# Kernel tuning notes

Hardware: AMD Instinct MI355X
Metric: run time of the kernel (lower is better)

## Reference

```python
import jax, jax.numpy as jnp
import numpy as np

B, S, D = 16, 2048, 128


def setup_inputs() -> dict:
    key = jax.random.key(0)
    kq, kk, kv, km = jax.random.split(key, 4)
    q = jax.random.normal(kq, (B, S, D), dtype=jnp.float32)
    k = jax.random.normal(kk, (B, S, D), dtype=jnp.float32)
    v = jax.random.normal(kv, (B, S, D), dtype=jnp.float32)
    mask = jax.random.randint(km, (B, S, S), 0, 2, dtype=jnp.int32)
    return {"q": q, "k": k, "v": v, "mask": mask}


def softmax_one(x):
    # repo's softmax_one: subtract max, denominator is 1 + sum(exp)
    x = x - jnp.max(x, axis=-1, keepdims=True)
    e = jnp.exp(x)
    return e / (1.0 + jnp.sum(e, axis=-1, keepdims=True))


def reference(q, k, v, mask):
    d_k = k.shape[-1]
    zero = jnp.zeros((q.shape[0], 1, d_k), dtype=q.dtype)
    # prepend zero 'sink' key/value token along the sequence axis
    k1 = jnp.concatenate([zero, k], axis=1)          # [B, S+1, D]
    v1 = jnp.concatenate([zero, v], axis=1)          # [B, S+1, D]
    scores = jnp.einsum('bqd,bkd->bqk', q, k1) / np.sqrt(d_k)  # [B, S, S+1]
    # F.pad(mask, (1, 0)) pads sink column with 0 -> sink score masked
    m = jnp.pad(mask, ((0, 0), (0, 0), (1, 0)))
    scores = jnp.where(m == 0, jnp.float32(-1e9), scores)
    p_attn = softmax_one(scores)                     # [B, S, S+1]
    out = jnp.einsum('bqk,bkd->bqd', p_attn, v1)     # [B, S, D]
    return (out, p_attn)
```

## Files before the change

kernel.cpp:

```cpp
#include <hip/hip_runtime.h>
#include <hip/hip_bf16.h>

typedef __attribute__((ext_vector_type(8))) __bf16 bf16x8;
typedef __attribute__((ext_vector_type(4))) __bf16 bf16x4;
typedef __attribute__((ext_vector_type(4))) float  f32x4;
typedef float f32x4u __attribute__((ext_vector_type(4), aligned(4)));

#define NB 16
#define NS 2048
#define ND 128
#define QT 64
#define KT 64
#define NKT (NS / KT)
#define SCALE 0.08838834764831845f

#define VMW12() asm volatile("s_waitcnt vmcnt(12)" ::: "memory")
#define VMW8()  asm volatile("s_waitcnt vmcnt(8)"  ::: "memory")
#define VMW4()  asm volatile("s_waitcnt vmcnt(4)"  ::: "memory")
#define SCHED0() __builtin_amdgcn_sched_barrier(0)
#define SBAR()  __builtin_amdgcn_s_barrier()

__device__ __forceinline__ bf16x8 ld8_256(const __bf16* base, int row, int byteInRow) {
    int off = row * 256 + (byteInRow ^ ((row & 7) << 4));
    return *reinterpret_cast<const bf16x8*>(reinterpret_cast<const char*>(base) + off);
}
__device__ __forceinline__ bf16x8 ld8_128(const __bf16* base, int row, int byteInRow) {
    int off = row * 128 + (byteInRow ^ ((row & 7) << 4));
    return *reinterpret_cast<const bf16x8*>(reinterpret_cast<const char*>(base) + off);
}
__device__ __forceinline__ void glds16(const void* g, void* l) {
    __builtin_amdgcn_global_load_lds(
        (const __attribute__((address_space(1))) unsigned int*)g,
        (__attribute__((address_space(3))) unsigned int*)l, 16, 0, 0);
}

__global__ __launch_bounds__(256) void conv_qk(const float* __restrict__ q,
                                               const float* __restrict__ k,
                                               __bf16* __restrict__ qb,
                                               __bf16* __restrict__ kb) {
    size_t i = (size_t)blockIdx.x * 256 + threadIdx.x;
    const float4* qs = (const float4*)q;
    const float4* ks = (const float4*)k;
    float4 a = qs[2 * i], b = qs[2 * i + 1];
    bf16x8 o;
    o[0] = (__bf16)(a.x * SCALE); o[1] = (__bf16)(a.y * SCALE);
    o[2] = (__bf16)(a.z * SCALE); o[3] = (__bf16)(a.w * SCALE);
    o[4] = (__bf16)(b.x * SCALE); o[5] = (__bf16)(b.y * SCALE);
    o[6] = (__bf16)(b.z * SCALE); o[7] = (__bf16)(b.w * SCALE);
    *(bf16x8*)&qb[i * 8] = o;
    a = ks[2 * i]; b = ks[2 * i + 1];
    o[0] = (__bf16)a.x; o[1] = (__bf16)a.y; o[2] = (__bf16)a.z; o[3] = (__bf16)a.w;
    o[4] = (__bf16)b.x; o[5] = (__bf16)b.y; o[6] = (__bf16)b.z; o[7] = (__bf16)b.w;
    *(bf16x8*)&kb[i * 8] = o;
}

__global__ __launch_bounds__(256) void conv_vt(const float* __restrict__ v,
                                               __bf16* __restrict__ vt) {
    __shared__ __bf16 tile[128 * 128];
    const int b = blockIdx.x >> 4, st = blockIdx.x & 15;
    const int s0 = st * 128, t = threadIdx.x;
    const int rlane = t >> 5, cv = (t & 31) * 4;
    #pragma unroll
    for (int it = 0; it < 16; ++it) {
        int s = rlane + it * 8;
        float4 f = *(const float4*)(v + ((size_t)b * NS + s0 + s) * ND + cv);
        bf16x4 h;
        h[0] = (__bf16)f.x; h[1] = (__bf16)f.y; h[2] = (__bf16)f.z; h[3] = (__bf16)f.w;
        *(bf16x4*)&tile[s * 128 + (cv ^ (s & 60))] = h;
    }
    __syncthreads();
    #pragma unroll
    for (int it = 0; it < 16; ++it) {
        int d = rlane + it * 8;
        bf16x4 o;
        #pragma unroll
        for (int e = 0; e < 4; ++e)
            o[e] = tile[(cv + e) * 128 + (d ^ ((cv + e) & 60))];
        *(bf16x4*)&vt[((size_t)b * ND + d) * NS + s0 + cv] = o;
    }
}

__global__ __launch_bounds__(256, 2) void qa_main(
    const __bf16* __restrict__ qb, const __bf16* __restrict__ kb,
    const __bf16* __restrict__ vtb, const int* __restrict__ mg,
    float* __restrict__ outg, float* __restrict__ pg)
{
    __shared__ __align__(16) char bufs[3][KT * ND * 2];
    __shared__ unsigned short bmt[NKT * 256];
    __shared__ __align__(16) __bf16 Ps[4][16 * KT];

    const int bid = blockIdx.x;
    const int lb  = (bid & 7) * 64 + (bid >> 3);
    const int b   = lb >> 5;
    const int q0  = (lb & 31) * QT;
    const int t   = threadIdx.x;
    const int w   = t >> 6;
    const int l15 = t & 15;
    const int g   = (t & 63) >> 4;
    const int myrow = w * 16 + l15;

    const __bf16* kbB  = kb  + (size_t)b * NS * ND;
    const __bf16* vtbB = vtb + (size_t)b * ND * NS;
    const int*    mrow = mg  + (size_t)(b * NS + q0 + myrow) * NS;

    if (t < QT) pg[(size_t)(b * NS + q0 + t) * (size_t)(NS + 1)] = 0.0f;

    bf16x8 qf[4];
    {
        const __bf16* qrow = qb + (size_t)(b * NS + q0 + myrow) * ND;
        #pragma unroll
        for (int kc = 0; kc < 4; ++kc)
            qf[kc] = *(const bf16x8*)(qrow + kc * 32 + g * 8);
    }

    auto stageK = [&](char* buf, int k0) {
        #pragma unroll
        for (int i = 0; i < 4; ++i) {
            int c = i * 256 + t;
            int row = c >> 4, pc = c & 15, lc = pc ^ (row & 7);
            glds16(kbB + (size_t)(k0 + row) * ND + lc * 8, buf + c * 16);
        }
    };
    auto stageV = [&](char* buf, int k0) {
        #pragma unroll
        for (int i = 0; i < 4; ++i) {
            int c = i * 256 + t;
            int d = c >> 3, pc = c & 7, lc = pc ^ (d & 7);
            glds16(vtbB + (size_t)d * NS + k0 + lc * 8, buf + c * 16);
        }
    };

    float mrun = -1e9f, srun = 0.0f;
    int4 mA[4], mB[4];

    stageK(bufs[0], 0);
    stageK(bufs[1], KT);
    #pragma unroll
    for (int c = 0; c < 4; ++c) mA[c] = *(const int4*)(mrow + c * 16 + g * 4);
    VMW8();
    SCHED0(); SBAR(); SCHED0();

    auto stepA = [&](int kt, const int4* mcur, int4* mnxt) {
        if (kt + 2 < NKT) stageK(bufs[(kt + 2) % 3], (kt + 2) * KT);
        if (kt + 1 < NKT) {
            #pragma unroll
            for (int c = 0; c < 4; ++c)
                mnxt[c] = *(const int4*)(mrow + (kt + 1) * KT + c * 16 + g * 4);
        }
        const __bf16* Kbuf = (const __bf16*)bufs[kt % 3];
        f32x4 acc[4];
        #pragma unroll
        for (int c = 0; c < 4; ++c) {
            f32x4 z = {0.f, 0.f, 0.f, 0.f}; acc[c] = z;
            #pragma unroll
            for (int kc = 0; kc < 4; ++kc) {
                bf16x8 kf = ld8_256(Kbuf, c * 16 + l15, kc * 64 + g * 16);
                acc[c] = __builtin_amdgcn_mfma_f32_16x16x32_bf16(kf, qf[kc], acc[c], 0, 0, 0);
            }
        }
        float sv[16]; unsigned bits = 0;
        #pragma unroll
        for (int c = 0; c < 4; ++c) {
            int mm[4] = {mcur[c].x, mcur[c].y, mcur[c].z, mcur[c].w};
            #pragma unroll
            for (int r = 0; r < 4; ++r) {
                bool on = mm[r] != 0;
                sv[c * 4 + r] = on ? acc[c][r] : -1e30f;
                bits |= on ? (1u << (c * 4 + r)) : 0u;
            }
        }
        float x0 = fmaxf(fmaxf(sv[0], sv[1]),  fmaxf(sv[2], sv[3]));
        float x1 = fmaxf(fmaxf(sv[4], sv[5]),  fmaxf(sv[6], sv[7]));
        float x2 = fmaxf(fmaxf(sv[8], sv[9]),  fmaxf(sv[10], sv[11]));
        float x3 = fmaxf(fmaxf(sv[12], sv[13]), fmaxf(sv[14], sv[15]));
        float mx = fmaxf(fmaxf(x0, x1), fmaxf(x2, x3));
        mx = fmaxf(mx, __shfl_xor(mx, 16));
        mx = fmaxf(mx, __shfl_xor(mx, 32));
        float mnew = fmaxf(mrun, mx);
        float e[16];
        #pragma unroll
        for (int i = 0; i < 16; ++i) e[i] = __expf(sv[i] - mnew);
        float p0 = (e[0] + e[1]) + (e[2] + e[3]);
        float p1 = (e[4] + e[5]) + (e[6] + e[7]);
        float p2 = (e[8] + e[9]) + (e[10] + e[11]);
        float p3 = (e[12] + e[13]) + (e[14] + e[15]);
        float ps = (p0 + p1) + (p2 + p3);
        ps += __shfl_xor(ps, 16);
        ps += __shfl_xor(ps, 32);
        srun = srun * __expf(mrun - mnew) + ps;
        mrun = mnew;
        bmt[kt * 256 + t] = (unsigned short)bits;
        if (kt <= NKT - 3)      { VMW12(); }
        else if (kt == NKT - 2) { VMW8();  }
        SCHED0(); SBAR(); SCHED0();
    };

    for (int kt = 0; kt < NKT; kt += 2) {
        stepA(kt,     mA, mB);
        stepA(kt + 1, mB, mA);
    }

    const float inv = 1.0f / (1.0f + srun);

    f32x4 oacc[8];
    #pragma unroll
    for (int cf = 0; cf < 8; ++cf) { f32x4 z = {0.f, 0.f, 0.f, 0.f}; oacc[cf] = z; }

    int iA = 0, iB = 1, iC = 2;
    stageK(bufs[0], 0);
    stageV(bufs[1], 0);
    VMW4();
    SCHED0(); SBAR(); SCHED0();

    const size_t prow = (size_t)(b * NS + q0 + myrow) * (size_t)(NS + 1);
    __bf16* Psw = Ps[w];

    for (int kt = 0; kt < NKT; ++kt) {
        const int k0 = kt * KT;
        if (kt + 1 < NKT) stageK(bufs[iC], k0 + KT);

        const __bf16* Kbuf = (const __bf16*)bufs[iA];
        f32x4 acc[4];
        #pragma unroll
        for (int c = 0; c < 4; ++c) {
            f32x4 z = {0.f, 0.f, 0.f, 0.f}; acc[c] = z;
            #pragma unroll
            for (int kc = 0; kc < 4; ++kc) {
                bf16x8 kf = ld8_256(Kbuf, c * 16 + l15, kc * 64 + g * 16);
                acc[c] = __builtin_amdgcn_mfma_f32_16x16x32_bf16(kf, qf[kc], acc[c], 0, 0, 0);
            }
        }

        unsigned bits = bmt[kt * 256 + t];
        #pragma unroll
        for (int c = 0; c < 4; ++c) {
            f32x4 pv; bf16x4 pb;
            #pragma unroll
            for (int r = 0; r < 4; ++r) {
                bool on = (bits >> (c * 4 + r)) & 1u;
                float p = on ? __expf(acc[c][r] - mrun) * inv : 0.0f;
                pv[r] = p; pb[r] = (__bf16)p;
            }
            *(f32x4u*)&pg[prow + 1 + k0 + c * 16 + g * 4] = pv;
            int off = l15 * 128 + ((c * 32 + g * 8) ^ ((l15 & 7) << 4));
            *(bf16x4*)((char*)Psw + off) = pb;
        }

        if (kt < NKT - 1) { VMW8(); } else { VMW4(); }
        SCHED0(); SBAR(); SCHED0();

        if (kt + 1 < NKT) stageV(bufs[iA], k0 + KT);

        const __bf16* Vbuf = (const __bf16*)bufs[iB];
        #pragma unroll
        for (int kc = 0; kc < 2; ++kc) {
            bf16x8 af = ld8_128(Psw, l15, kc * 64 + g * 16);
            #pragma unroll
            for (int cf = 0; cf < 8; ++cf) {
                bf16x8 vf = ld8_128(Vbuf, cf * 16 + l15, kc * 64 + g * 16);
                oacc[cf] = __builtin_amdgcn_mfma_f32_16x16x32_bf16(af, vf, oacc[cf], 0, 0, 0);
            }
        }

        if (kt < NKT - 1) { VMW8(); }
        SCHED0(); SBAR(); SCHED0();

        int nA = iC, nB = iA, nC = iB;
        iA = nA; iB = nB; iC = nC;
    }

    #pragma unroll
    for (int cf = 0; cf < 8; ++cf)
        #pragma unroll
        for (int r = 0; r < 4; ++r)
            outg[(size_t)(b * NS + q0 + w * 16 + g * 4 + r) * ND + cf * 16 + l15] = oacc[cf][r];
}

__device__ __forceinline__ void stage_rm(__bf16* dst, const float* src, int t) {
    int row = t >> 2, cg = t & 3;
    const float4* s4 = reinterpret_cast<const float4*>(src + (size_t)row * ND) + cg * 8;
    #pragma unroll
    for (int j = 0; j < 8; ++j) {
        float4 f = s4[j];
        bf16x4 h;
        h[0] = (__bf16)f.x; h[1] = (__bf16)f.y; h[2] = (__bf16)f.z; h[3] = (__bf16)f.w;
        int off = (cg * 64 + j * 8) ^ ((row & 7) << 4);
        *reinterpret_cast<bf16x4*>(reinterpret_cast<char*>(dst) + row * 256 + off) = h;
    }
}

__global__ __launch_bounds__(256, 2) void qa_fused_fb(
    const float* __restrict__ qg, const float* __restrict__ kg,
    const float* __restrict__ vg, const int* __restrict__ mg,
    float* __restrict__ outg, float* __restrict__ pg)
{
    __shared__ __bf16 Qs[QT * ND];
    __shared__ __bf16 Ks[KT * ND];
    __shared__ __bf16 Vt[ND * KT];
    __shared__ __bf16 Psf[4 * 16 * KT];
    __shared__ unsigned int bmf[QT][64];

    const int bid = blockIdx.x;
    const int lb  = (bid & 7) * 64 + (bid >> 3);
    const int b   = lb >> 5;
    const int q0  = (lb & 31) * QT;
    const int t   = threadIdx.x;
    const int w   = t >> 6;
    const int l   = t & 63;
    const int l15 = l & 15;
    const int g   = l >> 4;

    stage_rm(Qs, qg + ((size_t)b * NS + q0) * ND, t);
    if (t < QT) pg[((size_t)b * NS + q0 + t) * (size_t)(NS + 1)] = 0.0f;
    __syncthreads();

    bf16x8 qf[4];
    const int arow = w * 16 + l15;
    #pragma unroll
    for (int kc = 0; kc < 4; ++kc) qf[kc] = ld8_256(Qs, arow, kc * 64 + g * 16);

    float mrun[4], srun[4];
    #pragma unroll
    for (int r = 0; r < 4; ++r) { mrun[r] = -1e9f; srun[r] = 0.0f; }

    for (int kt = 0; kt < NKT; ++kt) {
        const int k0 = kt * KT;
        __syncthreads();
        stage_rm(Ks, kg + ((size_t)b * NS + k0) * ND, t);
        #pragma unroll 4
        for (int i = 0; i < 16; ++i) {
            int row = w * 16 + i;
            int mv = mg[((size_t)b * NS + (q0 + row)) * NS + k0 + l];
            unsigned long long bal = __ballot(mv != 0);
            if (l == 0) {
                bmf[row][2 * kt]     = (unsigned)bal;
                bmf[row][2 * kt + 1] = (unsigned)(bal >> 32);
            }
        }
        __syncthreads();

        f32x4 acc[4];
        #pragma unroll
        for (int c = 0; c < 4; ++c) {
            f32x4 z = {0.f, 0.f, 0.f, 0.f};
            acc[c] = z;
            #pragma unroll
            for (int kc = 0; kc < 4; ++kc) {
                bf16x8 bf = ld8_256(Ks, c * 16 + l15, kc * 64 + g * 16);
                acc[c] = __builtin_amdgcn_mfma_f32_16x16x32_bf16(qf[kc], bf, acc[c], 0, 0, 0);
            }
        }

        #pragma unroll
        for (int r = 0; r < 4; ++r) {
            const int row = w * 16 + g * 4 + r;
            const unsigned w0 = bmf[row][2 * kt], w1 = bmf[row][2 * kt + 1];
            float sv[4], tmax = -1e9f;
            #pragma unroll
            for (int c = 0; c < 4; ++c) {
                int cb = c * 16 + l15;
                unsigned word = (c < 2) ? w0 : w1;
                bool on = (word >> (cb & 31)) & 1u;
                float s = on ? acc[c][r] * SCALE : -1e9f;
                sv[c] = s;
                tmax = fmaxf(tmax, s);
            }
            #pragma unroll
            for (int d = 1; d < 16; d <<= 1) tmax = fmaxf(tmax, __shfl_xor(tmax, d));
            float mnew = fmaxf(mrun[r], tmax);
            float corr = __expf(mrun[r] - mnew);
            float ps = 0.f;
            #pragma unroll
            for (int c = 0; c < 4; ++c) ps += __expf(sv[c] - mnew);
            #pragma unroll
            for (int d = 1; d < 16; d <<= 1) ps += __shfl_xor(ps, d);
            srun[r] = srun[r] * corr + ps;
            mrun[r] = mnew;
        }
    }

    float inv[4];
    #pragma unroll
    for (int r = 0; r < 4; ++r) inv[r] = 1.0f / (1.0f + srun[r]);

    f32x4 oacc[8];
    #pragma unroll
    for (int cf = 0; cf < 8; ++cf) { f32x4 z = {0.f,0.f,0.f,0.f}; oacc[cf] = z; }

    __bf16* Psw = Psf + w * (16 * KT);

    for (int kt = 0; kt < NKT; ++kt) {
        const int k0 = kt * KT;
        __syncthreads();
        stage_rm(Ks, kg + ((size_t)b * NS + k0) * ND, t);
        {
            int kk = t >> 2, dg = t & 3;
            const float4* s4 = reinterpret_cast<const float4*>(vg + ((size_t)b * NS + k0 + kk) * ND) + dg * 8;
            #pragma unroll
            for (int j = 0; j < 8; ++j) {
                float4 f = s4[j];
                int d0 = dg * 32 + j * 4;
                float fv[4] = {f.x, f.y, f.z, f.w};
                #pragma unroll
                for (int e = 0; e < 4; ++e) {
                    int d = d0 + e;
                    int off = d * 128 + ((kk * 2) ^ ((d & 7) << 4));
                    *reinterpret_cast<__bf16*>(reinterpret_cast<char*>(Vt) + off) = (__bf16)fv[e];
                }
            }
        }
        __syncthreads();

        f32x4 acc[4];
        #pragma unroll
        for (int c = 0; c < 4; ++c) {
            f32x4 z = {0.f, 0.f, 0.f, 0.f};
            acc[c] = z;
            #pragma unroll
            for (int kc = 0; kc < 4; ++kc) {
                bf16x8 bf = ld8_256(Ks, c * 16 + l15, kc * 64 + g * 16);
                acc[c] = __builtin_amdgcn_mfma_f32_16x16x32_bf16(qf[kc], bf, acc[c], 0, 0, 0);
            }
        }

        #pragma unroll
        for (int r = 0; r < 4; ++r) {
            const int row16 = g * 4 + r;
            const int row = w * 16 + row16;
            const unsigned w0 = bmf[row][2 * kt], w1 = bmf[row][2 * kt + 1];
            const size_t prowf = ((size_t)b * NS + q0 + row) * (size_t)(NS + 1);
            #pragma unroll
            for (int c = 0; c < 4; ++c) {
                int cb = c * 16 + l15;
                unsigned word = (c < 2) ? w0 : w1;
                bool on = (word >> (cb & 31)) & 1u;
                float p = on ? __expf(acc[c][r] * SCALE - mrun[r]) * inv[r] : 0.0f;
                pg[prowf + 1 + k0 + cb] = p;
                int off = row16 * 128 + ((cb * 2) ^ ((row16 & 7) << 4));
                *reinterpret_cast<__bf16*>(reinterpret_cast<char*>(Psw) + off) = (__bf16)p;
            }
        }

        #pragma unroll
        for (int kc = 0; kc < 2; ++kc) {
            bf16x8 af = ld8_128(Psw, l15, kc * 64 + g * 16);
            #pragma unroll
            for (int cf = 0; cf < 8; ++cf) {
                bf16x8 vfr = ld8_128(Vt, cf * 16 + l15, kc * 64 + g * 16);
                oacc[cf] = __builtin_amdgcn_mfma_f32_16x16x32_bf16(af, vfr, oacc[cf], 0, 0, 0);
            }
        }
    }

    #pragma unroll
    for (int cf = 0; cf < 8; ++cf)
        #pragma unroll
        for (int r = 0; r < 4; ++r)
            outg[((size_t)b * NS + q0 + w * 16 + g * 4 + r) * ND + cf * 16 + l15] = oacc[cf][r];
}

extern "C" void kernel_launch(void* const* d_in, const int* in_sizes, int n_in,
                              void* d_out, int out_size, void* d_ws, size_t ws_size,
                              hipStream_t stream) {
    const float* q = (const float*)d_in[0];
    const float* k = (const float*)d_in[1];
    const float* v = (const float*)d_in[2];
    const int*  mk = (const int*)d_in[3];
    float* out = (float*)d_out;
    float* p   = out + (size_t)NB * NS * ND;

    const size_t elems = (size_t)NB * NS * ND;
    const size_t need  = elems * 2 * 3;

    if (ws_size >= need) {
        __bf16* qb = (__bf16*)d_ws;
        __bf16* kb = qb + elems;
        __bf16* vt = kb + elems;
        conv_qk<<<dim3((unsigned)(elems / 8 / 256)), dim3(256), 0, stream>>>(q, k, qb, kb);
        conv_vt<<<dim3(NB * 16), dim3(256), 0, stream>>>(v, vt);
        qa_main<<<dim3(NB * (NS / QT)), dim3(256), 0, stream>>>(qb, kb, vt, mk, out, p);
    } else {
        qa_fused_fb<<<dim3(NB * (NS / QT)), dim3(256), 0, stream>>>(q, k, v, mk, out, p);
    }
}
```

Baseline: 631.9 us.

## Split attention into stats, merge, and PV kernels with key-halves parallelism

Replaces the single two-pass fused kernel with separate kernels. The first computes masked softmax max/sum statistics over each half of the keys and writes mask bits to global memory. A merge kernel then combines the two halves' stats. The PV kernel recomputes scores, writes p_attn and accumulates partial outputs per key half, and a final add kernel sums the two halves. This doubles the grid size to raise occupancy and parallelism and uses smaller key tiles. The cost is extra launches, global round-trips for bits, stats and partial outputs, and a larger workspace requirement.

```diff
diff --git a/kernel.cpp b/kernel.cpp
--- a/kernel.cpp
+++ b/kernel.cpp
@@ -9,23 +9,14 @@
 #define NB 16
 #define NS 2048
 #define ND 128
-#define QT 64
-#define KT 64
-#define NKT (NS / KT)
 #define SCALE 0.08838834764831845f
 
-#define VMW12() asm volatile("s_waitcnt vmcnt(12)" ::: "memory")
-#define VMW8()  asm volatile("s_waitcnt vmcnt(8)"  ::: "memory")
-#define VMW4()  asm volatile("s_waitcnt vmcnt(4)"  ::: "memory")
+#define VMW(n) asm volatile("s_waitcnt vmcnt(" #n ")" ::: "memory")
 #define SCHED0() __builtin_amdgcn_sched_barrier(0)
 #define SBAR()  __builtin_amdgcn_s_barrier()
 
 __device__ __forceinline__ bf16x8 ld8_256(const __bf16* base, int row, int byteInRow) {
     int off = row * 256 + (byteInRow ^ ((row & 7) << 4));
-    return *reinterpret_cast<const bf16x8*>(reinterpret_cast<const char*>(base) + off);
-}
-__device__ __forceinline__ bf16x8 ld8_128(const __bf16* base, int row, int byteInRow) {
-    int off = row * 128 + (byteInRow ^ ((row & 7) << 4));
     return *reinterpret_cast<const bf16x8*>(reinterpret_cast<const char*>(base) + off);
 }
 __device__ __forceinline__ void glds16(const void* g, void* l) {
@@ -80,202 +71,238 @@
     }
 }
 
-__global__ __launch_bounds__(256, 2) void qa_main(
-    const __bf16* __restrict__ qb, const __bf16* __restrict__ kb,
-    const __bf16* __restrict__ vtb, const int* __restrict__ mg,
-    float* __restrict__ outg, float* __restrict__ pg)
+__global__ __launch_bounds__(256, 4) void kA_ms(
+    const __bf16* __restrict__ qbuf, const __bf16* __restrict__ kbuf,
+    const int* __restrict__ mg, unsigned short* __restrict__ bitsg,
+    float* __restrict__ msb)
 {
-    __shared__ __align__(16) char bufs[3][KT * ND * 2];
-    __shared__ unsigned short bmt[NKT * 256];
-    __shared__ __align__(16) __bf16 Ps[4][16 * KT];
-
+    __shared__ __align__(16) char bufs[3][32 * 256];
     const int bid = blockIdx.x;
-    const int lb  = (bid & 7) * 64 + (bid >> 3);
-    const int b   = lb >> 5;
-    const int q0  = (lb & 31) * QT;
-    const int t   = threadIdx.x;
-    const int w   = t >> 6;
-    const int l15 = t & 15;
-    const int g   = (t & 63) >> 4;
-    const int myrow = w * 16 + l15;
-
-    const __bf16* kbB  = kb  + (size_t)b * NS * ND;
-    const __bf16* vtbB = vtb + (size_t)b * ND * NS;
-    const int*    mrow = mg  + (size_t)(b * NS + q0 + myrow) * NS;
-
-    if (t < QT) pg[(size_t)(b * NS + q0 + t) * (size_t)(NS + 1)] = 0.0f;
+    const int lb = (bid & 7) * 128 + (bid >> 3);
+    const int b = lb >> 6, qblk = (lb >> 1) & 31, kh = lb & 1;
+    const int t = threadIdx.x, w = t >> 6, l15 = t & 15, g = (t & 63) >> 4;
+    const int qrow = qblk * 64 + w * 16 + l15;
+    const size_t grow = (size_t)b * NS + qrow;
+    const int kbase = kh * 1024;
+    const __bf16* kbB = kbuf + (size_t)b * NS * ND;
+    const int* mrow = mg + grow * NS + kbase;
 
     bf16x8 qf[4];
     {
-        const __bf16* qrow = qb + (size_t)(b * NS + q0 + myrow) * ND;
-        #pragma unroll
-        for (int kc = 0; kc < 4; ++kc)
-            qf[kc] = *(const bf16x8*)(qrow + kc * 32 + g * 8);
-    }
-
-    auto stageK = [&](char* buf, int k0) {
-        #pragma unroll
-        for (int i = 0; i < 4; ++i) {
-            int c = i * 256 + t;
-            int row = c >> 4, pc = c & 15, lc = pc ^ (row & 7);
+        const __bf16* qr = qbuf + grow * ND;
+        #pragma unroll
+        for (int kc = 0; kc < 4; ++kc) qf[kc] = *(const bf16x8*)(qr + kc * 32 + g * 8);
+    }
+    auto stageK = [&](char* buf, int j) {
+        const int k0 = kbase + j * 32;
+        #pragma unroll
+        for (int i = 0; i < 2; ++i) {
+            int c = i * 256 + t, row = c >> 4, pc = c & 15, lc = pc ^ (row & 7);
             glds16(kbB + (size_t)(k0 + row) * ND + lc * 8, buf + c * 16);
         }
     };
-    auto stageV = [&](char* buf, int k0) {
-        #pragma unroll
-        for (int i = 0; i < 4; ++i) {
-            int c = i * 256 + t;
-            int d = c >> 3, pc = c & 7, lc = pc ^ (d & 7);
-            glds16(vtbB + (size_t)d * NS + k0 + lc * 8, buf + c * 16);
-        }
-    };
-
-    float mrun = -1e9f, srun = 0.0f;
-    int4 mA[4], mB[4];
 
     stageK(bufs[0], 0);
-    stageK(bufs[1], KT);
-    #pragma unroll
-    for (int c = 0; c < 4; ++c) mA[c] = *(const int4*)(mrow + c * 16 + g * 4);
-    VMW8();
-    SCHED0(); SBAR(); SCHED0();
-
-    auto stepA = [&](int kt, const int4* mcur, int4* mnxt) {
-        if (kt + 2 < NKT) stageK(bufs[(kt + 2) % 3], (kt + 2) * KT);
-        if (kt + 1 < NKT) {
-            #pragma unroll
-            for (int c = 0; c < 4; ++c)
-                mnxt[c] = *(const int4*)(mrow + (kt + 1) * KT + c * 16 + g * 4);
-        }
-        const __bf16* Kbuf = (const __bf16*)bufs[kt % 3];
-        f32x4 acc[4];
-        #pragma unroll
-        for (int c = 0; c < 4; ++c) {
+    stageK(bufs[1], 1);
+    int4 mk[2][2];
+    #pragma unroll
+    for (int c = 0; c < 2; ++c) mk[0][c] = *(const int4*)(mrow + c * 16 + g * 4);
+
+    float ml = -1e30f, sl = 0.0f;
+    unsigned bitsArr[8];
+    #pragma unroll
+    for (int p = 0; p < 8; ++p) bitsArr[p] = 0u;
+
+    #pragma unroll
+    for (int i = 0; i < 32; ++i) {
+        if (i == 0 || i == 31) { VMW(4); } else { VMW(6); }
+        SCHED0(); SBAR(); SCHED0();
+        const __bf16* K = (const __bf16*)bufs[i % 3];
+        f32x4 acc[2];
+        #pragma unroll
+        for (int c = 0; c < 2; ++c) {
             f32x4 z = {0.f, 0.f, 0.f, 0.f}; acc[c] = z;
             #pragma unroll
             for (int kc = 0; kc < 4; ++kc) {
-                bf16x8 kf = ld8_256(Kbuf, c * 16 + l15, kc * 64 + g * 16);
+                bf16x8 kf = ld8_256(K, c * 16 + l15, kc * 64 + g * 16);
                 acc[c] = __builtin_amdgcn_mfma_f32_16x16x32_bf16(kf, qf[kc], acc[c], 0, 0, 0);
             }
         }
-        float sv[16]; unsigned bits = 0;
-        #pragma unroll
-        for (int c = 0; c < 4; ++c) {
-            int mm[4] = {mcur[c].x, mcur[c].y, mcur[c].z, mcur[c].w};
+        const int4* mc = mk[i & 1];
+        unsigned bits = 0; float mx = -1e30f; float sv[8]; bool onv[8];
+        #pragma unroll
+        for (int c = 0; c < 2; ++c) {
+            int mm[4] = {mc[c].x, mc[c].y, mc[c].z, mc[c].w};
             #pragma unroll
             for (int r = 0; r < 4; ++r) {
                 bool on = mm[r] != 0;
-                sv[c * 4 + r] = on ? acc[c][r] : -1e30f;
+                sv[c * 4 + r] = acc[c][r];
+                onv[c * 4 + r] = on;
+                mx = fmaxf(mx, on ? acc[c][r] : -1e30f);
                 bits |= on ? (1u << (c * 4 + r)) : 0u;
             }
         }
-        float x0 = fmaxf(fmaxf(sv[0], sv[1]),  fmaxf(sv[2], sv[3]));
-        float x1 = fmaxf(fmaxf(sv[4], sv[5]),  fmaxf(sv[6], sv[7]));
-        float x2 = fmaxf(fmaxf(sv[8], sv[9]),  fmaxf(sv[10], sv[11]));
-        float x3 = fmaxf(fmaxf(sv[12], sv[13]), fmaxf(sv[14], sv[15]));
-        float mx = fmaxf(fmaxf(x0, x1), fmaxf(x2, x3));
-        mx = fmaxf(mx, __shfl_xor(mx, 16));
-        mx = fmaxf(mx, __shfl_xor(mx, 32));
-        float mnew = fmaxf(mrun, mx);
-        float e[16];
-        #pragma unroll
-        for (int i = 0; i < 16; ++i) e[i] = __expf(sv[i] - mnew);
-        float p0 = (e[0] + e[1]) + (e[2] + e[3]);
-        float p1 = (e[4] + e[5]) + (e[6] + e[7]);
-        float p2 = (e[8] + e[9]) + (e[10] + e[11]);
-        float p3 = (e[12] + e[13]) + (e[14] + e[15]);
-        float ps = (p0 + p1) + (p2 + p3);
-        ps += __shfl_xor(ps, 16);
-        ps += __shfl_xor(ps, 32);
-        srun = srun * __expf(mrun - mnew) + ps;
-        mrun = mnew;
-        bmt[kt * 256 + t] = (unsigned short)bits;
-        if (kt <= NKT - 3)      { VMW12(); }
-        else if (kt == NKT - 2) { VMW8();  }
+        float mnew = fmaxf(ml, mx);
+        float corr = __expf(ml - mnew);
+        float ps = 0.f;
+        #pragma unroll
+        for (int q = 0; q < 8; ++q) ps += onv[q] ? __expf(sv[q] - mnew) : 0.f;
+        sl = sl * corr + ps;
+        ml = mnew;
+        bitsArr[i >> 2] |= bits << ((i & 3) * 8);
+        if (i + 2 < 32) stageK(bufs[(i + 2) % 3], i + 2);
+        if (i + 1 < 32) {
+            #pragma unroll
+            for (int c = 0; c < 2; ++c)
+                mk[(i + 1) & 1][c] = *(const int4*)(mrow + (i + 1) * 32 + c * 16 + g * 4);
+        }
+    }
+    #pragma unroll
+    for (int d = 16; d <= 32; d <<= 1) {
+        float mo = __shfl_xor(ml, d), so = __shfl_xor(sl, d);
+        float mn = fmaxf(ml, mo);
+        sl = sl * __expf(ml - mn) + so * __expf(mo - mn);
+        ml = mn;
+    }
+    uint4 b0 = {bitsArr[0], bitsArr[1], bitsArr[2], bitsArr[3]};
+    uint4 b1 = {bitsArr[4], bitsArr[5], bitsArr[6], bitsArr[7]};
+    uint4* bp = (uint4*)(bitsg + (grow * 4 + g) * 32 + kh * 16);
+    bp[0] = b0; bp[1] = b1;
+    if (g == 0) ((float2*)msb)[grow * 2 + kh] = make_float2(ml, sl);
+}
+
+__global__ __launch_bounds__(256) void kM_merge(const float* __restrict__ msb,
+                                                float* __restrict__ minv,
+                                                float* __restrict__ pg)
+{
+    int r = blockIdx.x * 256 + threadIdx.x;
+    float4 ms = ((const float4*)msb)[r];
+    float m = fmaxf(ms.x, ms.z);
+    float s = ms.y * __expf(ms.x - m) + ms.w * __expf(ms.z - m);
+    float inv = 1.0f / (1.0f + s);
+    ((float2*)minv)[r] = make_float2(m, inv);
+    pg[(size_t)r * (NS + 1)] = 0.0f;
+}
+
+__global__ __launch_bounds__(256, 4) void kB_pv(
+    const __bf16* __restrict__ qbuf, const __bf16* __restrict__ kbuf,
+    const __bf16* __restrict__ vtb, const unsigned short* __restrict__ bitsg,
+    const float* __restrict__ minv, float* __restrict__ pg,
+    float* __restrict__ outp)
+{
+    __shared__ __align__(16) char Kb[2][32 * 256];
+    __shared__ __align__(16) char Vb[2][128 * 64];
+    __shared__ __align__(16) __bf16 Ps[4][16 * 32];
+    const int bid = blockIdx.x;
+    const int lb = (bid & 7) * 128 + (bid >> 3);
+    const int b = lb >> 6, qblk = (lb >> 1) & 31, kh = lb & 1;
+    const int q0 = qblk * 64;
+    const int t = threadIdx.x, w = t >> 6, l15 = t & 15, g = (t & 63) >> 4;
+    const int qrow = q0 + w * 16 + l15;
+    const size_t grow = (size_t)b * NS + qrow;
+    const int kbase = kh * 1024;
+    const __bf16* kbB  = kbuf + (size_t)b * NS * ND;
+    const __bf16* vtbB = vtb  + (size_t)b * ND * NS;
+
+    float2 mi = ((const float2*)minv)[grow];
+    bf16x8 qf[4];
+    {
+        const __bf16* qr = qbuf + grow * ND;
+        #pragma unroll
+        for (int kc = 0; kc < 4; ++kc) qf[kc] = *(const bf16x8*)(qr + kc * 32 + g * 8);
+    }
+    auto stageK = [&](char* buf, int j) {
+        const int k0 = kbase + j * 32;
+        #pragma unroll
+        for (int i = 0; i < 2; ++i) {
+            int c = i * 256 + t, row = c >> 4, pc = c & 15, lc = pc ^ (row & 7);
+            glds16(kbB + (size_t)(k0 + row) * ND + lc * 8, buf + c * 16);
+        }
+    };
+    auto stageV = [&](char* buf, int j) {
+        const int k0 = kbase + j * 32;
+        #pragma unroll
+        for (int i = 0; i < 2; ++i) {
+            int c = i * 256 + t, d = c >> 2, pc = c & 3;
+            glds16(vtbB + (size_t)d * NS + k0 + pc * 8, buf + c * 16);
+        }
+    };
+
+    f32x4 oacc[8];
+    #pragma unroll
+    for (int cf = 0; cf < 8; ++cf) { f32x4 z = {0.f, 0.f, 0.f, 0.f}; oacc[cf] = z; }
+
+    stageK(Kb[0], 0);
+    stageV(Vb[0], 0);
+    const size_t prow = grow * (size_t)(NS + 1);
+    const unsigned short* bitp = bitsg + (grow * 4 + g) * 32 + kh * 16;
+    __bf16* Psw = Ps[w];
+
+    for (int j = 0; j < 32; ++j) {
+        const int k0 = kbase + j * 32;
+        if (j < 31) stageK(Kb[(j + 1) & 1], j + 1);
+        unsigned bits = *(volatile const unsigned short*)(bitp + (j >> 1));
+        if (j == 0)       { VMW(5); }
+        else if (j == 31) { VMW(6); }
+        else              { VMW(8); }
         SCHED0(); SBAR(); SCHED0();
-    };
-
-    for (int kt = 0; kt < NKT; kt += 2) {
-        stepA(kt,     mA, mB);
-        stepA(kt + 1, mB, mA);
-    }
-
-    const float inv = 1.0f / (1.0f + srun);
-
-    f32x4 oacc[8];
-    #pragma unroll
-    for (int cf = 0; cf < 8; ++cf) { f32x4 z = {0.f, 0.f, 0.f, 0.f}; oacc[cf] = z; }
-
-    int iA = 0, iB = 1, iC = 2;
-    stageK(bufs[0], 0);
-    stageV(bufs[1], 0);
-    VMW4();
-    SCHED0(); SBAR(); SCHED0();
-
-    const size_t prow = (size_t)(b * NS + q0 + myrow) * (size_t)(NS + 1);
-    __bf16* Psw = Ps[w];
-
-    for (int kt = 0; kt < NKT; ++kt) {
-        const int k0 = kt * KT;
-        if (kt + 1 < NKT) stageK(bufs[iC], k0 + KT);
-
-        const __bf16* Kbuf = (const __bf16*)bufs[iA];
-        f32x4 acc[4];
-        #pragma unroll
-        for (int c = 0; c < 4; ++c) {
+        const __bf16* K = (const __bf16*)Kb[j & 1];
+        f32x4 acc[2];
+        #pragma unroll
+        for (int c = 0; c < 2; ++c) {
             f32x4 z = {0.f, 0.f, 0.f, 0.f}; acc[c] = z;
             #pragma unroll
             for (int kc = 0; kc < 4; ++kc) {
-                bf16x8 kf = ld8_256(Kbuf, c * 16 + l15, kc * 64 + g * 16);
+                bf16x8 kf = ld8_256(K, c * 16 + l15, kc * 64 + g * 16);
                 acc[c] = __builtin_amdgcn_mfma_f32_16x16x32_bf16(kf, qf[kc], acc[c], 0, 0, 0);
             }
         }
-
-        unsigned bits = bmt[kt * 256 + t];
-        #pragma unroll
-        for (int c = 0; c < 4; ++c) {
+        const int sh = (j & 1) * 8;
+        #pragma unroll
+        for (int c = 0; c < 2; ++c) {
             f32x4 pv; bf16x4 pb;
             #pragma unroll
             for (int r = 0; r < 4; ++r) {
-                bool on = (bits >> (c * 4 + r)) & 1u;
-                float p = on ? __expf(acc[c][r] - mrun) * inv : 0.0f;
+                bool on = (bits >> (sh + c * 4 + r)) & 1u;
+                float p = on ? __expf(acc[c][r] - mi.x) * mi.y : 0.0f;
                 pv[r] = p; pb[r] = (__bf16)p;
             }
             *(f32x4u*)&pg[prow + 1 + k0 + c * 16 + g * 4] = pv;
-            int off = l15 * 128 + ((c * 32 + g * 8) ^ ((l15 & 7) << 4));
-            *(bf16x4*)((char*)Psw + off) = pb;
-        }
-
-        if (kt < NKT - 1) { VMW8(); } else { VMW4(); }
+            *(bf16x4*)((char*)Psw + l15 * 64 + c * 32 + g * 8) = pb;
+        }
+        if (j < 31) stageV(Vb[(j + 1) & 1], j + 1);
+        if (j == 31) { VMW(3); } else { VMW(7); }
         SCHED0(); SBAR(); SCHED0();
-
-        if (kt + 1 < NKT) stageV(bufs[iA], k0 + KT);
-
-        const __bf16* Vbuf = (const __bf16*)bufs[iB];
-        #pragma unroll
-        for (int kc = 0; kc < 2; ++kc) {
-            bf16x8 af = ld8_128(Psw, l15, kc * 64 + g * 16);
-            #pragma unroll
-            for (int cf = 0; cf < 8; ++cf) {
-                bf16x8 vf = ld8_128(Vbuf, cf * 16 + l15, kc * 64 + g * 16);
-                oacc[cf] = __builtin_amdgcn_mfma_f32_16x16x32_bf16(af, vf, oacc[cf], 0, 0, 0);
-            }
-        }
-
-        if (kt < NKT - 1) { VMW8(); }
-        SCHED0(); SBAR(); SCHED0();
-
-        int nA = iC, nB = iA, nC = iB;
-        iA = nA; iB = nB; iC = nC;
-    }
-
+        const char* V = Vb[j & 1];
+        bf16x8 af = *(const bf16x8*)((const char*)Psw + l15 * 64 + g * 16);
+        #pragma unroll
+        for (int cf = 0; cf < 8; ++cf) {
+            bf16x8 vf = *(const bf16x8*)(V + (cf * 16 + l15) * 64 + g * 16);
+            oacc[cf] = __builtin_amdgcn_mfma_f32_16x16x32_bf16(af, vf, oacc[cf], 0, 0, 0);
+        }
+    }
+
+    float* op = outp + (size_t)kh * NB * NS * ND;
     #pragma unroll
     for (int cf = 0; cf < 8; ++cf)
         #pragma unroll
         for (int r = 0; r < 4; ++r)
-            outg[(size_t)(b * NS + q0 + w * 16 + g * 4 + r) * ND + cf * 16 + l15] = oacc[cf][r];
-}
-
+            op[((size_t)b * NS + q0 + w * 16 + g * 4 + r) * ND + cf * 16 + l15] = oacc[cf][r];
+}
+
+__global__ __launch_bounds__(256) void kC_add(const float* __restrict__ outp,
+                                              float* __restrict__ outg)
+{
+    size_t i = (size_t)blockIdx.x * 256 + threadIdx.x;
+    const f32x4* a = (const f32x4*)outp;
+    f32x4 r = a[i] + a[i + (size_t)NB * NS * ND / 4];
+    ((f32x4*)outg)[i] = r;
+}
+
+__device__ __forceinline__ bf16x8 ld8_128(const __bf16* base, int row, int byteInRow) {
+    int off = row * 128 + (byteInRow ^ ((row & 7) << 4));
+    return *reinterpret_cast<const bf16x8*>(reinterpret_cast<const char*>(base) + off);
+}
 __device__ __forceinline__ void stage_rm(__bf16* dst, const float* src, int t) {
     int row = t >> 2, cg = t & 3;
     const float4* s4 = reinterpret_cast<const float4*>(src + (size_t)row * ND) + cg * 8;
@@ -294,16 +321,16 @@
     const float* __restrict__ vg, const int* __restrict__ mg,
     float* __restrict__ outg, float* __restrict__ pg)
 {
-    __shared__ __bf16 Qs[QT * ND];
-    __shared__ __bf16 Ks[KT * ND];
-    __shared__ __bf16 Vt[ND * KT];
-    __shared__ __bf16 Psf[4 * 16 * KT];
-    __shared__ unsigned int bmf[QT][64];
+    __shared__ __bf16 Qs[64 * ND];
+    __shared__ __bf16 Ks[64 * ND];
+    __shared__ __bf16 Vt[ND * 64];
+    __shared__ __bf16 Psf[4 * 16 * 64];
+    __shared__ unsigned int bmf[64][64];
 
     const int bid = blockIdx.x;
     const int lb  = (bid & 7) * 64 + (bid >> 3);
     const int b   = lb >> 5;
-    const int q0  = (lb & 31) * QT;
+    const int q0  = (lb & 31) * 64;
     const int t   = threadIdx.x;
     const int w   = t >> 6;
     const int l   = t & 63;
@@ -311,7 +338,7 @@
     const int g   = l >> 4;
 
     stage_rm(Qs, qg + ((size_t)b * NS + q0) * ND, t);
-    if (t < QT) pg[((size_t)b * NS + q0 + t) * (size_t)(NS + 1)] = 0.0f;
+    if (t < 64) pg[((size_t)b * NS + q0 + t) * (size_t)(NS + 1)] = 0.0f;
     __syncthreads();
 
     bf16x8 qf[4];
@@ -323,8 +350,8 @@
     #pragma unroll
     for (int r = 0; r < 4; ++r) { mrun[r] = -1e9f; srun[r] = 0.0f; }
 
-    for (int kt = 0; kt < NKT; ++kt) {
-        const int k0 = kt * KT;
+    for (int kt = 0; kt < 32; ++kt) {
+        const int k0 = kt * 64;
         __syncthreads();
         stage_rm(Ks, kg + ((size_t)b * NS + k0) * ND, t);
         #pragma unroll 4
@@ -387,10 +414,10 @@
     #pragma unroll
     for (int cf = 0; cf < 8; ++cf) { f32x4 z = {0.f,0.f,0.f,0.f}; oacc[cf] = z; }
 
-    __bf16* Psw = Psf + w * (16 * KT);
-
-    for (int kt = 0; kt < NKT; ++kt) {
-        const int k0 = kt * KT;
+    __bf16* Psw = Psf + w * (16 * 64);
+
+    for (int kt = 0; kt < 32; ++kt) {
+        const int k0 = kt * 64;
         __syncthreads();
         stage_rm(Ks, kg + ((size_t)b * NS + k0) * ND, t);
         {
@@ -469,17 +496,33 @@
     float* out = (float*)d_out;
     float* p   = out + (size_t)NB * NS * ND;
 
-    const size_t elems = (size_t)NB * NS * ND;
-    const size_t need  = elems * 2 * 3;
+    const size_t E = (size_t)NB * NS * ND;
+    const size_t off_qb   = 0;
+    const size_t off_kb   = 2 * E;
+    const size_t off_vt   = 4 * E;
+    const size_t off_bits = 6 * E;
+    const size_t off_msb  = 8 * E;
+    const size_t off_minv = 8 * E + 524288;
+    const size_t off_outp = 8 * E + 786432;
+    const size_t need     = 16 * E + 786432;
 
     if (ws_size >= need) {
-        __bf16* qb = (__bf16*)d_ws;
-        __bf16* kb = qb + elems;
-        __bf16* vt = kb + elems;
-        conv_qk<<<dim3((unsigned)(elems / 8 / 256)), dim3(256), 0, stream>>>(q, k, qb, kb);
+        char* ws = (char*)d_ws;
+        __bf16* qb = (__bf16*)(ws + off_qb);
+        __bf16* kb = (__bf16*)(ws + off_kb);
+        __bf16* vt = (__bf16*)(ws + off_vt);
+        unsigned short* bits = (unsigned short*)(ws + off_bits);
+        float* msb  = (float*)(ws + off_msb);
+        float* minv = (float*)(ws + off_minv);
+        float* outp = (float*)(ws + off_outp);
+
+        conv_qk<<<dim3((unsigned)(E / 8 / 256)), dim3(256), 0, stream>>>(q, k, qb, kb);
         conv_vt<<<dim3(NB * 16), dim3(256), 0, stream>>>(v, vt);
-        qa_main<<<dim3(NB * (NS / QT)), dim3(256), 0, stream>>>(qb, kb, vt, mk, out, p);
+        kA_ms<<<dim3(1024), dim3(256), 0, stream>>>(qb, kb, mk, bits, msb);
+        kM_merge<<<dim3(NB * NS / 256), dim3(256), 0, stream>>>(msb, minv, p);
+        kB_pv<<<dim3(1024), dim3(256), 0, stream>>>(qb, kb, vt, bits, minv, p, outp);
+        kC_add<<<dim3((unsigned)(E / 4 / 256)), dim3(256), 0, stream>>>(outp, out);
     } else {
-        qa_fused_fb<<<dim3(NB * (NS / QT)), dim3(256), 0, stream>>>(q, k, v, mk, out, p);
-    }
-}
+        qa_fused_fb<<<dim3(NB * (NS / 64)), dim3(256), 0, stream>>>(q, k, v, mk, out, p);
+    }
+}
```

Result: slower. 652.4 us (+3.2%).
